# Performance work log

Hardware: AMD Instinct MI355X
Metric: run time of the kernel (lower is better)

Reference implementation:

```python
import jax, jax.numpy as jnp
import numpy as np

DIM = 1024
HEADS = 16
HEAD_DIM = DIM // HEADS
HIDDEN = 4 * DIM
EPS = 1e-5


def _layernorm(x, g, b):
    m = jnp.mean(x, axis=-1, keepdims=True)
    v = jnp.mean((x - m) ** 2, axis=-1, keepdims=True)
    return (x - m) * jax.lax.rsqrt(v + EPS) * g + b


def setup_inputs() -> dict:
    key = jax.random.key(0)
    ks = jax.random.split(key, 8)
    s = 0.02
    return {
        "x": jax.random.normal(ks[0], (16, 577, DIM), dtype=jnp.float32),
        "w_qkv": jax.random.normal(ks[1], (3 * DIM, DIM), dtype=jnp.float32) * s,
        "b_qkv": jnp.zeros((3 * DIM,), dtype=jnp.float32),
        "w_proj": jax.random.normal(ks[2], (DIM, DIM), dtype=jnp.float32) * s,
        "b_proj": jnp.zeros((DIM,), dtype=jnp.float32),
        "ln1_g": jnp.ones((DIM,), dtype=jnp.float32),
        "ln1_b": jnp.zeros((DIM,), dtype=jnp.float32),
        "ln2_g": jnp.ones((DIM,), dtype=jnp.float32),
        "ln2_b": jnp.zeros((DIM,), dtype=jnp.float32),
        "w_fc1": jax.random.normal(ks[3], (HIDDEN, DIM), dtype=jnp.float32) * s,
        "b_fc1": jnp.zeros((HIDDEN,), dtype=jnp.float32),
        "w_fc2": jax.random.normal(ks[4], (DIM, HIDDEN), dtype=jnp.float32) * s,
        "b_fc2": jnp.zeros((DIM,), dtype=jnp.float32),
    }


def reference(x, w_qkv, b_qkv, w_proj, b_proj, ln1_g, ln1_b, ln2_g, ln2_b,
              w_fc1, b_fc1, w_fc2, b_fc2):
    B, N, C = x.shape
    scale = HEAD_DIM ** -0.5
    # --- attention sub-block ---
    xn = _layernorm(x, ln1_g, ln1_b)
    qkv = xn @ w_qkv.T + b_qkv  # [B, N, 3C]
    qkv = qkv.reshape(B, N, 3, HEADS, HEAD_DIM)
    q = qkv[:, :, 0].transpose(0, 2, 1, 3)  # [B, H, N, D]
    k = qkv[:, :, 1].transpose(0, 2, 1, 3)
    v = qkv[:, :, 2].transpose(0, 2, 1, 3)
    attn = jnp.einsum('bhnd,bhmd->bhnm', q, k) * scale
    attn = jax.nn.softmax(attn, axis=-1)
    y = jnp.einsum('bhnm,bhmd->bhnd', attn, v)  # [B, H, N, D]
    y = y.transpose(0, 2, 1, 3).reshape(B, N, C)
    y = y @ w_proj.T + b_proj
    x = x + y
    # --- MLP sub-block ---
    xn2 = _layernorm(x, ln2_g, ln2_b)
    h = jax.nn.gelu(xn2 @ w_fc1.T + b_fc1, approximate=False)
    x = x + (h @ w_fc2.T + b_fc2)
    return x
```

## Files before the change

kernel.cpp:

```cpp
#include <hip/hip_runtime.h>
#include <cmath>


#define MTOK 9232
#define MPAD 9344
#define MT_TILES 73
#define SEQ  577
#define SEQP 640
#define NKT  10

typedef _Float16 half8  __attribute__((ext_vector_type(8)));
typedef _Float16 half4  __attribute__((ext_vector_type(4)));
typedef float    float4v __attribute__((ext_vector_type(4)));

__device__ __forceinline__ void gl_lds16(const void* g, void* l) {
  __builtin_amdgcn_global_load_lds((const __attribute__((address_space(1))) void*)g,
                                   (__attribute__((address_space(3))) void*)l, 16, 0, 0);
}

__device__ __forceinline__ float fexp2(float x) { return __builtin_amdgcn_exp2f(x); }
__device__ __forceinline__ float frcp(float x)  { return __builtin_amdgcn_rcpf(x); }

__global__ __launch_bounds__(256) void cvt_all_kernel(const float* __restrict__ s0, _Float16* __restrict__ d0,
                                                      const float* __restrict__ s1, _Float16* __restrict__ d1,
                                                      const float* __restrict__ s2, _Float16* __restrict__ d2,
                                                      const float* __restrict__ s3, _Float16* __restrict__ d3) {
  int blk = blockIdx.x;
  const float* in; _Float16* out; int base;
  if (blk < 1536)      { in = s0; out = d0; base = blk; }
  else if (blk < 2048) { in = s1; out = d1; base = blk - 1536; }
  else if (blk < 4096) { in = s2; out = d2; base = blk - 2048; }
  else                 { in = s3; out = d3; base = blk - 4096; }
  int i = (base * 256 + threadIdx.x) * 8;
  float4v a = *(const float4v*)(in + i);
  float4v b = *(const float4v*)(in + i + 4);
  half8 o = { (_Float16)a[0], (_Float16)a[1], (_Float16)a[2], (_Float16)a[3],
              (_Float16)b[0], (_Float16)b[1], (_Float16)b[2], (_Float16)b[3] };
  *(half8*)(out + i) = o;
}

__global__ __launch_bounds__(256) void ln_kernel(const float* __restrict__ x,
                                                 const float* __restrict__ gam,
                                                 const float* __restrict__ bet,
                                                 _Float16* __restrict__ out, int mrows) {
  int row = blockIdx.x, t = threadIdx.x;
  _Float16* orow = out + (long)row * 1024 + t * 4;
  if (row >= mrows) { half4 z = {}; *(half4*)orow = z; return; }
  float4v xv = *(const float4v*)(x + (long)row * 1024 + t * 4);
  float s  = xv[0] + xv[1] + xv[2] + xv[3];
  float ss = xv[0]*xv[0] + xv[1]*xv[1] + xv[2]*xv[2] + xv[3]*xv[3];
  #pragma unroll
  for (int o = 32; o > 0; o >>= 1) { s += __shfl_down(s, o); ss += __shfl_down(ss, o); }
  __shared__ float red[8];
  int w = t >> 6;
  if ((t & 63) == 0) { red[w] = s; red[4 + w] = ss; }
  __syncthreads();
  s  = red[0] + red[1] + red[2] + red[3];
  ss = red[4] + red[5] + red[6] + red[7];
  float mean = s * (1.0f / 1024.0f);
  float var  = ss * (1.0f / 1024.0f) - mean * mean;
  float rstd = rsqrtf(var + 1e-5f);
  float4v gv = *(const float4v*)(gam + t * 4);
  float4v bv = *(const float4v*)(bet + t * 4);
  half4 o;
  #pragma unroll
  for (int i = 0; i < 4; i++) o[i] = (_Float16)((xv[i] - mean) * rstd * gv[i] + bv[i]);
  *(half4*)orow = o;
}

template <int EPI>
__global__ __launch_bounds__(256, 3) void gemm_bt(const _Float16* __restrict__ A,
                                                  const _Float16* __restrict__ Bw,
                                                  const float* __restrict__ bias,
                                                  const float* __restrict__ res,
                                                  void* __restrict__ outv, int Ndim, int K) {
  __shared__ __align__(16) _Float16 SH[16384];
  _Float16* As = SH;
  _Float16* Bs = SH + 8192;
  const int GM = 16;
  int nTiles = Ndim >> 7;
  int per = GM * nTiles;
  int lin = blockIdx.x;
  int panel = lin / per;
  int rem = lin - panel * per;
  int gm = MT_TILES - panel * GM; if (gm > GM) gm = GM;
  int mt = panel * GM + rem % gm;
  int nt = rem / gm;
  int t = threadIdx.x, w = t >> 6, l = t & 63;
  int wm = (w >> 1) * 64, wn = (w & 1) * 64;
  int g = l >> 4, li = l & 15;
  float4v acc[4][4] = {};

  long soff[4];
  #pragma unroll
  for (int r = 0; r < 4; ++r) {
    int idx = (w * 4 + r) * 64 + l;
    int row = idx >> 3;
    int kc  = (idx & 7) ^ (row & 7);
    soff[r] = (long)row * K + kc * 8;
  }
  int aro[2][4], bro[2][4];
  #pragma unroll
  for (int ks = 0; ks < 2; ++ks) {
    #pragma unroll
    for (int i = 0; i < 4; ++i) {
      int ar = wm + i * 16 + li;
      aro[ks][i] = ar * 64 + (((ks * 4 + g) ^ (ar & 7)) * 8);
      int br = wn + i * 16 + li;
      bro[ks][i] = br * 64 + (((ks * 4 + g) ^ (br & 7)) * 8);
    }
  }

  const _Float16* ak = A  + (long)mt * 128 * K;
  const _Float16* bk = Bw + (long)nt * 128 * K;
  int nk = K >> 6;
  for (int kt = 0; kt < nk; ++kt) {
    #pragma unroll
    for (int r = 0; r < 4; ++r) {
      gl_lds16(ak + soff[r], As + (w * 4 + r) * 512);
      gl_lds16(bk + soff[r], Bs + (w * 4 + r) * 512);
    }
    ak += 64; bk += 64;
    __syncthreads();
    #pragma unroll
    for (int ks = 0; ks < 2; ++ks) {
      half8 af[4], bf[4];
      #pragma unroll
      for (int i = 0; i < 4; i++) af[i] = *(const half8*)(As + aro[ks][i]);
      #pragma unroll
      for (int j = 0; j < 4; j++) bf[j] = *(const half8*)(Bs + bro[ks][j]);
      #pragma unroll
      for (int i = 0; i < 4; i++)
        #pragma unroll
        for (int j = 0; j < 4; j++)
          acc[i][j] = __builtin_amdgcn_mfma_f32_16x16x32_f16(af[i], bf[j], acc[i][j], 0, 0, 0);
    }
    __syncthreads();
  }
  if (EPI == 2) {
    float* Shf = (float*)SH;
    #pragma unroll
    for (int p = 0; p < 4; ++p) {
      if ((w & 1) == (p >> 1)) {
        int j0 = (p & 1) * 2;
        #pragma unroll
        for (int i = 0; i < 4; ++i) {
          #pragma unroll
          for (int jj = 0; jj < 2; ++jj) {
            #pragma unroll
            for (int r = 0; r < 4; ++r) {
              int row = wm + i * 16 + g * 4 + r;
              Shf[row * 36 + jj * 16 + li] = acc[i][j0 + jj][r];
            }
          }
        }
      }
      __syncthreads();
      #pragma unroll
      for (int it = 0; it < 4; ++it) {
        int chunk = it * 256 + t;
        int row = chunk >> 3, c4 = chunk & 7;
        int grow = mt * 128 + row;
        if (grow < MTOK) {
          float4v v = *(const float4v*)(Shf + row * 36 + c4 * 4);
          int gcol = nt * 128 + p * 32 + c4 * 4;
          float4v bv = *(const float4v*)(bias + gcol);
          float4v rv = *(const float4v*)(res + (long)grow * Ndim + gcol);
          v = v + bv + rv;
          *(float4v*)((float*)outv + (long)grow * Ndim + gcol) = v;
        }
      }
      __syncthreads();
    }
  } else {
    _Float16* Sh = SH;
    float bsv[4];
    #pragma unroll
    for (int j = 0; j < 4; ++j) bsv[j] = bias[nt * 128 + wn + j * 16 + li];
    #pragma unroll
    for (int p = 0; p < 2; ++p) {
      if ((w & 1) == p) {
        #pragma unroll
        for (int i = 0; i < 4; ++i) {
          int rl = (w >> 1) * 64 + i * 16 + g * 4;
          #pragma unroll
          for (int j = 0; j < 4; ++j) {
            #pragma unroll
            for (int r = 0; r < 4; ++r) {
              float v = acc[i][j][r] + bsv[j];
              if (EPI == 1) {
                float y = v * (0.79788456f + 0.035677408f * v * v);
                v = v * frcp(1.0f + fexp2(-2.88539008f * y));
              }
              Sh[(rl + r) * 68 + j * 16 + li] = (_Float16)v;
            }
          }
        }
      }
      __syncthreads();
      #pragma unroll
      for (int cc = 0; cc < 4; ++cc) {
        int chunk = cc * 256 + t;
        int row = chunk >> 3, kc8 = chunk & 7;
        half8 hv = *(const half8*)(Sh + row * 68 + kc8 * 8);
        *(half8*)((_Float16*)outv + (long)(mt * 128 + row) * Ndim + nt * 128 + p * 64 + kc8 * 8) = hv;
      }
      __syncthreads();
    }
  }
}

__global__ __launch_bounds__(256) void vt_kernel(const _Float16* __restrict__ qkv,
                                                 _Float16* __restrict__ Vt) {
  int kt = blockIdx.x, bh = blockIdx.y;
  int b = bh >> 4, h = bh & 15;
  long base = (long)b * SEQ;
  __shared__ _Float16 Lt[64][72];
  int t = threadIdx.x;
  #pragma unroll
  for (int c = t; c < 512; c += 256) {
    int key = c >> 3, dc = c & 7;
    int kglob = kt * 64 + key;
    half8 v = {};
    if (kglob < SEQ) v = *(const half8*)(qkv + (base + kglob) * 3072 + 2048 + h * 64 + dc * 8);
    *(half8*)(&Lt[key][dc * 8]) = v;
  }
  __syncthreads();
  #pragma unroll
  for (int c = t; c < 512; c += 256) {
    int d = c >> 3, kc = c & 7;
    half8 o;
    #pragma unroll
    for (int j = 0; j < 8; j++) o[j] = Lt[kc * 8 + j][d];
    *(half8*)(Vt + ((long)bh * 64 + d) * SEQP + kt * 64 + kc * 8) = o;
  }
}

__global__ __launch_bounds__(256) void attn_kernel(const _Float16* __restrict__ qkv,
                                                   const _Float16* __restrict__ Vt,
                                                   _Float16* __restrict__ Y) {
  int qt = blockIdx.x, bh = blockIdx.y;
  int b = bh >> 4, h = bh & 15;
  long base = (long)b * SEQ;
  int t = threadIdx.x, w = t >> 6, l = t & 63;
  int g = l >> 4, li = l & 15;
  __shared__ __align__(16) _Float16 Ks[64 * 64];
  __shared__ __align__(16) _Float16 Vs[64 * 64];
  __shared__ __align__(16) _Float16 Pw[4][32 * 72];
  int q0 = qt * 128 + w * 32;
  half8 qf[2][2];
  #pragma unroll
  for (int m = 0; m < 2; ++m)
    #pragma unroll
    for (int ks = 0; ks < 2; ++ks)
      qf[m][ks] = *(const half8*)(qkv + (base + q0 + m * 16 + li) * 3072 + h * 64 + ks * 32 + g * 8);
  float4v o[2][4] = {};
  float mrow[2][4] = { { -1e30f, -1e30f, -1e30f, -1e30f }, { -1e30f, -1e30f, -1e30f, -1e30f } };
  float lrow[2][4] = {};
  const _Float16* vtb = Vt + (long)bh * 64 * SEQP;
  for (int kt = 0; kt < NKT; ++kt) {
    #pragma unroll
    for (int rr = 0; rr < 2; ++rr) {
      int idx = rr * 256 + w * 64 + l;
      int row = idx >> 3;
      int kc  = (idx & 7) ^ (row & 7);
      gl_lds16(qkv + (base + kt * 64 + row) * 3072 + 1024 + h * 64 + kc * 8,
               Ks + (rr * 256 + w * 64) * 8);
      gl_lds16(vtb + (long)row * SEQP + kt * 64 + kc * 8,
               Vs + (rr * 256 + w * 64) * 8);
    }
    __syncthreads();
    float4v s[2][4] = {};
    #pragma unroll
    for (int ks = 0; ks < 2; ++ks) {
      #pragma unroll
      for (int n = 0; n < 4; ++n) {
        int kr = n * 16 + li;
        half8 kf = *(const half8*)(Ks + kr * 64 + (((ks * 4 + g) ^ (kr & 7)) * 8));
        s[0][n] = __builtin_amdgcn_mfma_f32_16x16x32_f16(qf[0][ks], kf, s[0][n], 0, 0, 0);
        s[1][n] = __builtin_amdgcn_mfma_f32_16x16x32_f16(qf[1][ks], kf, s[1][n], 0, 0, 0);
      }
    }
    bool last = (kt == NKT - 1);
    const float sc = 0.125f * 1.44269504f;
    #pragma unroll
    for (int m = 0; m < 2; ++m) {
      #pragma unroll
      for (int r = 0; r < 4; ++r) {
        float v[4];
        #pragma unroll
        for (int n = 0; n < 4; ++n) {
          v[n] = s[m][n][r] * sc;
          if (last && (kt * 64 + n * 16 + li) >= SEQ) v[n] = -1e30f;
        }
        float a = fmaxf(fmaxf(v[0], v[1]), fmaxf(v[2], v[3]));
        a = fmaxf(a, __shfl_xor(a, 1));
        a = fmaxf(a, __shfl_xor(a, 2));
        a = fmaxf(a, __shfl_xor(a, 4));
        a = fmaxf(a, __shfl_xor(a, 8));
        float mn = fmaxf(mrow[m][r], a);
        float al = fexp2(mrow[m][r] - mn);
        mrow[m][r] = mn;
        int prow = m * 16 + g * 4 + r;
        float rs = 0.f;
        #pragma unroll
        for (int n = 0; n < 4; ++n) {
          float p = fexp2(v[n] - mn);
          rs += p;
          Pw[w][prow * 72 + n * 16 + li] = (_Float16)p;
        }
        rs += __shfl_xor(rs, 1);
        rs += __shfl_xor(rs, 2);
        rs += __shfl_xor(rs, 4);
        rs += __shfl_xor(rs, 8);
        lrow[m][r] = lrow[m][r] * al + rs;
        #pragma unroll
        for (int n = 0; n < 4; ++n) o[m][n][r] *= al;
      }
    }
    #pragma unroll
    for (int ks = 0; ks < 2; ++ks) {
      half8 pa[2];
      #pragma unroll
      for (int m = 0; m < 2; ++m)
        pa[m] = *(const half8*)(&Pw[w][(m * 16 + li) * 72 + ks * 32 + g * 8]);
      #pragma unroll
      for (int n = 0; n < 4; ++n) {
        int vr = n * 16 + li;
        half8 vf = *(const half8*)(Vs + vr * 64 + (((ks * 4 + g) ^ (vr & 7)) * 8));
        o[0][n] = __builtin_amdgcn_mfma_f32_16x16x32_f16(pa[0], vf, o[0][n], 0, 0, 0);
        o[1][n] = __builtin_amdgcn_mfma_f32_16x16x32_f16(pa[1], vf, o[1][n], 0, 0, 0);
      }
    }
    __syncthreads();
  }
  #pragma unroll
  for (int m = 0; m < 2; ++m) {
    #pragma unroll
    for (int r = 0; r < 4; ++r) {
      int qr = q0 + m * 16 + g * 4 + r;
      if (qr < SEQ) {
        float inv = frcp(lrow[m][r]);
        _Float16* yp = Y + (base + qr) * 1024 + h * 64 + li;
        #pragma unroll
        for (int n = 0; n < 4; ++n) yp[n * 16] = (_Float16)(o[m][n][r] * inv);
      }
    }
  }
}

extern "C" void kernel_launch(void* const* d_in, const int* in_sizes, int n_in,
                              void* d_out, int out_size, void* d_ws, size_t ws_size,
                              hipStream_t stream) {
  (void)in_sizes; (void)n_in; (void)out_size; (void)ws_size;
  const float* x      = (const float*)d_in[0];
  const float* w_qkv  = (const float*)d_in[1];
  const float* b_qkv  = (const float*)d_in[2];
  const float* w_proj = (const float*)d_in[3];
  const float* b_proj = (const float*)d_in[4];
  const float* ln1_g  = (const float*)d_in[5];
  const float* ln1_b  = (const float*)d_in[6];
  const float* ln2_g  = (const float*)d_in[7];
  const float* ln2_b  = (const float*)d_in[8];
  const float* w_fc1  = (const float*)d_in[9];
  const float* b_fc1  = (const float*)d_in[10];
  const float* w_fc2  = (const float*)d_in[11];
  const float* b_fc2  = (const float*)d_in[12];

  char* ws = (char*)d_ws;
  _Float16* Abuf = (_Float16*)ws;
  _Float16* Wq   = (_Float16*)(ws + 19136512);
  _Float16* Wp   = Wq + 3072 * 1024;
  _Float16* W1   = Wp + 1024 * 1024;
  _Float16* W2   = W1 + 4096 * 1024;
  _Float16* Qb   = (_Float16*)(ws + 44302336);
  _Float16* Yb   = Qb + (long)MPAD * 3072;
  _Float16* Hb   = Qb;
  float*    X1   = (float*)(ws + 120848384);
  _Float16* Vtb  = (_Float16*)(ws + 120848384);

  cvt_all_kernel<<<6144, 256, 0, stream>>>(w_qkv, Wq, w_proj, Wp, w_fc1, W1, w_fc2, W2);

  ln_kernel<<<MPAD, 256, 0, stream>>>(x, ln1_g, ln1_b, Abuf, MTOK);
  gemm_bt<0><<<73 * 24, 256, 0, stream>>>(Abuf, Wq, b_qkv, nullptr, Qb, 3072, 1024);
  vt_kernel<<<dim3(NKT, 256), 256, 0, stream>>>(Qb, Vtb);
  attn_kernel<<<dim3(5, 256), 256, 0, stream>>>(Qb, Vtb, Yb);
  gemm_bt<2><<<73 * 8, 256, 0, stream>>>(Yb, Wp, b_proj, x, X1, 1024, 1024);
  ln_kernel<<<MPAD, 256, 0, stream>>>(X1, ln2_g, ln2_b, Abuf, MTOK);
  gemm_bt<1><<<73 * 32, 256, 0, stream>>>(Abuf, W1, b_fc1, nullptr, Hb, 4096, 1024);
  gemm_bt<2><<<73 * 8, 256, 0, stream>>>(Hb, W2, b_fc2, X1, d_out, 1024, 4096);
}
```

Baseline: 545.4 us.

## Restructure attention to transposed S tiles, smaller query tiles, more blocks

The attention kernel now computes S transposed (K as the A operand), so each lane holds one query column and the row max and sum need only two cross-group shuffles. The softmax rescale factors are broadcast to the output layout with ds_bpermute. Probabilities are packed with cvt_pkrtz into a smaller per-wave LDS tile. Each wave now owns 16 queries instead of 32 and blocks cover 64 queries, doubling the grid to 2560 blocks with bh as the fast index and an occupancy hint of 4. The aim is less shuffle and exp overhead and better latency hiding, at the cost of loading each K/V tile twice as often per query and halving MFMA reuse of each K/V fragment.

```diff
diff --git a/kernel.cpp b/kernel.cpp
--- a/kernel.cpp
+++ b/kernel.cpp
@@ -11,6 +11,8 @@
 
 typedef _Float16 half8  __attribute__((ext_vector_type(8)));
 typedef _Float16 half4  __attribute__((ext_vector_type(4)));
+typedef _Float16 half2v __attribute__((ext_vector_type(2)));
+typedef __fp16   fp16x2 __attribute__((ext_vector_type(2)));
 typedef float    float4v __attribute__((ext_vector_type(4)));
 
 __device__ __forceinline__ void gl_lds16(const void* g, void* l) {
@@ -20,6 +22,13 @@
 
 __device__ __forceinline__ float fexp2(float x) { return __builtin_amdgcn_exp2f(x); }
 __device__ __forceinline__ float frcp(float x)  { return __builtin_amdgcn_rcpf(x); }
+__device__ __forceinline__ float bperm_f(int addr, float v) {
+  return __int_as_float(__builtin_amdgcn_ds_bpermute(addr, __float_as_int(v)));
+}
+__device__ __forceinline__ half2v pack2(float a, float b) {
+  fp16x2 p = __builtin_amdgcn_cvt_pkrtz(a, b);
+  return __builtin_bit_cast(half2v, p);
+}
 
 __global__ __launch_bounds__(256) void cvt_all_kernel(const float* __restrict__ s0, _Float16* __restrict__ d0,
                                                       const float* __restrict__ s1, _Float16* __restrict__ d1,
@@ -236,28 +245,27 @@
   }
 }
 
-__global__ __launch_bounds__(256) void attn_kernel(const _Float16* __restrict__ qkv,
-                                                   const _Float16* __restrict__ Vt,
-                                                   _Float16* __restrict__ Y) {
-  int qt = blockIdx.x, bh = blockIdx.y;
+__global__ __launch_bounds__(256, 4) void attn_kernel(const _Float16* __restrict__ qkv,
+                                                      const _Float16* __restrict__ Vt,
+                                                      _Float16* __restrict__ Y) {
+  int bh = blockIdx.x, qt = blockIdx.y;
   int b = bh >> 4, h = bh & 15;
   long base = (long)b * SEQ;
   int t = threadIdx.x, w = t >> 6, l = t & 63;
   int g = l >> 4, li = l & 15;
   __shared__ __align__(16) _Float16 Ks[64 * 64];
   __shared__ __align__(16) _Float16 Vs[64 * 64];
-  __shared__ __align__(16) _Float16 Pw[4][32 * 72];
-  int q0 = qt * 128 + w * 32;
-  half8 qf[2][2];
-  #pragma unroll
-  for (int m = 0; m < 2; ++m)
-    #pragma unroll
-    for (int ks = 0; ks < 2; ++ks)
-      qf[m][ks] = *(const half8*)(qkv + (base + q0 + m * 16 + li) * 3072 + h * 64 + ks * 32 + g * 8);
-  float4v o[2][4] = {};
-  float mrow[2][4] = { { -1e30f, -1e30f, -1e30f, -1e30f }, { -1e30f, -1e30f, -1e30f, -1e30f } };
-  float lrow[2][4] = {};
+  __shared__ __align__(16) _Float16 Pw[4][16 * 40];
+  int q0 = qt * 64 + w * 16;
+  half8 qf[2];
+  #pragma unroll
+  for (int ks = 0; ks < 2; ++ks)
+    qf[ks] = *(const half8*)(qkv + (base + q0 + li) * 3072 + h * 64 + ks * 32 + g * 8);
+  float4v o[4] = {};
+  float mold = -1e30f, lsum = 0.f;
+  int abase = (l & 48);
   const _Float16* vtb = Vt + (long)bh * 64 * SEQP;
+  const float sc = 0.125f * 1.44269504f;
   for (int kt = 0; kt < NKT; ++kt) {
     #pragma unroll
     for (int rr = 0; rr < 2; ++rr) {
@@ -270,81 +278,84 @@
                Vs + (rr * 256 + w * 64) * 8);
     }
     __syncthreads();
-    float4v s[2][4] = {};
+    float4v st[4] = {};
     #pragma unroll
     for (int ks = 0; ks < 2; ++ks) {
       #pragma unroll
-      for (int n = 0; n < 4; ++n) {
-        int kr = n * 16 + li;
+      for (int mt = 0; mt < 4; ++mt) {
+        int kr = mt * 16 + li;
         half8 kf = *(const half8*)(Ks + kr * 64 + (((ks * 4 + g) ^ (kr & 7)) * 8));
-        s[0][n] = __builtin_amdgcn_mfma_f32_16x16x32_f16(qf[0][ks], kf, s[0][n], 0, 0, 0);
-        s[1][n] = __builtin_amdgcn_mfma_f32_16x16x32_f16(qf[1][ks], kf, s[1][n], 0, 0, 0);
+        st[mt] = __builtin_amdgcn_mfma_f32_16x16x32_f16(kf, qf[ks], st[mt], 0, 0, 0);
       }
     }
     bool last = (kt == NKT - 1);
-    const float sc = 0.125f * 1.44269504f;
-    #pragma unroll
-    for (int m = 0; m < 2; ++m) {
+    float mx = -1e30f;
+    #pragma unroll
+    for (int mt = 0; mt < 4; ++mt) {
       #pragma unroll
       for (int r = 0; r < 4; ++r) {
-        float v[4];
-        #pragma unroll
-        for (int n = 0; n < 4; ++n) {
-          v[n] = s[m][n][r] * sc;
-          if (last && (kt * 64 + n * 16 + li) >= SEQ) v[n] = -1e30f;
-        }
-        float a = fmaxf(fmaxf(v[0], v[1]), fmaxf(v[2], v[3]));
-        a = fmaxf(a, __shfl_xor(a, 1));
-        a = fmaxf(a, __shfl_xor(a, 2));
-        a = fmaxf(a, __shfl_xor(a, 4));
-        a = fmaxf(a, __shfl_xor(a, 8));
-        float mn = fmaxf(mrow[m][r], a);
-        float al = fexp2(mrow[m][r] - mn);
-        mrow[m][r] = mn;
-        int prow = m * 16 + g * 4 + r;
-        float rs = 0.f;
-        #pragma unroll
-        for (int n = 0; n < 4; ++n) {
-          float p = fexp2(v[n] - mn);
-          rs += p;
-          Pw[w][prow * 72 + n * 16 + li] = (_Float16)p;
-        }
-        rs += __shfl_xor(rs, 1);
-        rs += __shfl_xor(rs, 2);
-        rs += __shfl_xor(rs, 4);
-        rs += __shfl_xor(rs, 8);
-        lrow[m][r] = lrow[m][r] * al + rs;
-        #pragma unroll
-        for (int n = 0; n < 4; ++n) o[m][n][r] *= al;
-      }
-    }
+        float v = st[mt][r] * sc;
+        if (last && (kt * 64 + mt * 16 + g * 4 + r) >= SEQ) v = -1e30f;
+        st[mt][r] = v;
+        mx = fmaxf(mx, v);
+      }
+    }
+    mx = fmaxf(mx, __shfl_xor(mx, 16));
+    mx = fmaxf(mx, __shfl_xor(mx, 32));
+    float mnew = fmaxf(mold, mx);
+    float alpha = fexp2(mold - mnew);
+    mold = mnew;
+    half2v pk[4][2];
+    float psum = 0.f;
+    #pragma unroll
+    for (int mt = 0; mt < 4; ++mt) {
+      float p0 = fexp2(st[mt][0] - mnew);
+      float p1 = fexp2(st[mt][1] - mnew);
+      float p2 = fexp2(st[mt][2] - mnew);
+      float p3 = fexp2(st[mt][3] - mnew);
+      psum += (p0 + p1) + (p2 + p3);
+      pk[mt][0] = pack2(p0, p1);
+      pk[mt][1] = pack2(p2, p3);
+    }
+    lsum = lsum * alpha + psum;
+    float ab[4];
+    #pragma unroll
+    for (int r = 0; r < 4; ++r) ab[r] = bperm_f(abase + 4 * r, alpha);
+    #pragma unroll
+    for (int nd = 0; nd < 4; ++nd)
+      #pragma unroll
+      for (int r = 0; r < 4; ++r) o[nd][r] *= ab[r];
     #pragma unroll
     for (int ks = 0; ks < 2; ++ks) {
-      half8 pa[2];
-      #pragma unroll
-      for (int m = 0; m < 2; ++m)
-        pa[m] = *(const half8*)(&Pw[w][(m * 16 + li) * 72 + ks * 32 + g * 8]);
-      #pragma unroll
-      for (int n = 0; n < 4; ++n) {
-        int vr = n * 16 + li;
+      #pragma unroll
+      for (int mtl = 0; mtl < 2; ++mtl) {
+        int mt = 2 * ks + mtl;
+        *(half2v*)(&Pw[w][li * 40 + mtl * 16 + g * 4])     = pk[mt][0];
+        *(half2v*)(&Pw[w][li * 40 + mtl * 16 + g * 4 + 2]) = pk[mt][1];
+      }
+      half8 pa = *(const half8*)(&Pw[w][li * 40 + g * 8]);
+      #pragma unroll
+      for (int nd = 0; nd < 4; ++nd) {
+        int vr = nd * 16 + li;
         half8 vf = *(const half8*)(Vs + vr * 64 + (((ks * 4 + g) ^ (vr & 7)) * 8));
-        o[0][n] = __builtin_amdgcn_mfma_f32_16x16x32_f16(pa[0], vf, o[0][n], 0, 0, 0);
-        o[1][n] = __builtin_amdgcn_mfma_f32_16x16x32_f16(pa[1], vf, o[1][n], 0, 0, 0);
+        o[nd] = __builtin_amdgcn_mfma_f32_16x16x32_f16(pa, vf, o[nd], 0, 0, 0);
       }
     }
     __syncthreads();
   }
-  #pragma unroll
-  for (int m = 0; m < 2; ++m) {
-    #pragma unroll
-    for (int r = 0; r < 4; ++r) {
-      int qr = q0 + m * 16 + g * 4 + r;
-      if (qr < SEQ) {
-        float inv = frcp(lrow[m][r]);
-        _Float16* yp = Y + (base + qr) * 1024 + h * 64 + li;
-        #pragma unroll
-        for (int n = 0; n < 4; ++n) yp[n * 16] = (_Float16)(o[m][n][r] * inv);
-      }
+  lsum += __shfl_xor(lsum, 16);
+  lsum += __shfl_xor(lsum, 32);
+  float linv = frcp(lsum);
+  float lb[4];
+  #pragma unroll
+  for (int r = 0; r < 4; ++r) lb[r] = bperm_f(abase + 4 * r, linv);
+  #pragma unroll
+  for (int r = 0; r < 4; ++r) {
+    int qr = qt * 64 + w * 16 + g * 4 + r;
+    if (qr < SEQ) {
+      _Float16* yp = Y + (base + qr) * 1024 + h * 64 + li;
+      #pragma unroll
+      for (int nd = 0; nd < 4; ++nd) yp[nd * 16] = (_Float16)(o[nd][r] * lb[r]);
     }
   }
 }
@@ -384,7 +395,7 @@
   ln_kernel<<<MPAD, 256, 0, stream>>>(x, ln1_g, ln1_b, Abuf, MTOK);
   gemm_bt<0><<<73 * 24, 256, 0, stream>>>(Abuf, Wq, b_qkv, nullptr, Qb, 3072, 1024);
   vt_kernel<<<dim3(NKT, 256), 256, 0, stream>>>(Qb, Vtb);
-  attn_kernel<<<dim3(5, 256), 256, 0, stream>>>(Qb, Vtb, Yb);
+  attn_kernel<<<dim3(256, NKT), 256, 0, stream>>>(Qb, Vtb, Yb);
   gemm_bt<2><<<73 * 8, 256, 0, stream>>>(Yb, Wp, b_proj, x, X1, 1024, 1024);
   ln_kernel<<<MPAD, 256, 0, stream>>>(X1, ln2_g, ln2_b, Abuf, MTOK);
   gemm_bt<1><<<73 * 32, 256, 0, stream>>>(Abuf, W1, b_fc1, nullptr, Hb, 4096, 1024);
```

New measurement: 513.9 us. 1.06x faster.
